# Kernel tuning notes

Measured on AMD Instinct MI355X. Metric: run time of the kernel, lower is better.

## Reference

```python
import jax, jax.numpy as jnp
import numpy as np

HEADS = 4
HID = 32
IN_CH = 3
N = 50000
E = 800000


def setup_inputs() -> dict:
    key = jax.random.key(0)
    ks = jax.random.split(key, 16)
    d1 = HEADS * HID  # 128
    s = 0.1
    inp = {
        'x': jax.random.normal(ks[0], (N, IN_CH), jnp.float32),
        'edge_index': jax.random.randint(ks[1], (2, E), 0, N, jnp.int64),
        # layer 1: in=3 -> heads*hid
        'W1': jax.random.normal(ks[2], (IN_CH, d1), jnp.float32) * s,
        'as1': jax.random.normal(ks[3], (HEADS, HID), jnp.float32) * s,
        'ad1': jax.random.normal(ks[4], (HEADS, HID), jnp.float32) * s,
        'b1': jnp.zeros((d1,), jnp.float32),
        # layer 2: 128 -> 128
        'W2': jax.random.normal(ks[5], (d1, d1), jnp.float32) * s,
        'as2': jax.random.normal(ks[6], (HEADS, HID), jnp.float32) * s,
        'ad2': jax.random.normal(ks[7], (HEADS, HID), jnp.float32) * s,
        'b2': jnp.zeros((d1,), jnp.float32),
        # layer 3: 128 -> 128
        'W3': jax.random.normal(ks[8], (d1, d1), jnp.float32) * s,
        'as3': jax.random.normal(ks[9], (HEADS, HID), jnp.float32) * s,
        'ad3': jax.random.normal(ks[10], (HEADS, HID), jnp.float32) * s,
        'b3': jnp.zeros((d1,), jnp.float32),
        # classifier: 128 -> 1
        'cW': jax.random.normal(ks[11], (d1, 1), jnp.float32) * s,
        'cb': jnp.zeros((1,), jnp.float32),
    }
    return inp


def _gat_layer(x, src, dst, n, W, a_s, a_d, b):
    """PyG GATConv (concat=True, negative_slope=0.2, self-loops already added)."""
    xp = (x @ W).reshape(n, HEADS, HID)              # [N,H,C]
    al_s = jnp.einsum('nhc,hc->nh', xp, a_s)          # [N,H]
    al_d = jnp.einsum('nhc,hc->nh', xp, a_d)          # [N,H]
    e = jax.nn.leaky_relu(al_s[src] + al_d[dst], 0.2)  # [E',H]
    emax = jax.ops.segment_max(e, dst, num_segments=n)  # segment softmax over dst
    ex = jnp.exp(e - emax[dst])
    den = jax.ops.segment_sum(ex, dst, num_segments=n)
    alpha = ex / (den[dst] + 1e-16)                   # [E',H]
    msg = xp[src] * alpha[:, :, None]                 # [E',H,C]
    out = jax.ops.segment_sum(msg, dst, num_segments=n)  # [N,H,C]
    return out.reshape(n, HEADS * HID) + b


def reference(x, edge_index, W1, as1, ad1, b1, W2, as2, ad2, b2, W3, as3, ad3, b3, cW, cb):
    n = x.shape[0]
    loops = jnp.arange(n, dtype=edge_index.dtype)
    src = jnp.concatenate([edge_index[0], loops])     # add self-loops (PyG default)
    dst = jnp.concatenate([edge_index[1], loops])
    h = jax.nn.elu(_gat_layer(x, src, dst, n, W1, as1, ad1, b1))
    h = jax.nn.elu(_gat_layer(h, src, dst, n, W2, as2, ad2, b2))
    h = jax.nn.elu(_gat_layer(h, src, dst, n, W3, as3, ad3, b3))
    logits = (h @ cW + cb)[:, 0]                      # [N]
    return jax.nn.sigmoid(logits)                     # eval mode output
```

## Files before the change

kernel.cpp:

```cpp
#include <hip/hip_runtime.h>
#include <math.h>

typedef unsigned int uint_t;
typedef __attribute__((ext_vector_type(8))) short bf16x8;
typedef __attribute__((ext_vector_type(4))) float f32x4;

#define BK_SHIFT 7
#define BK_NODES 128
#define MAXBK 512
#define PART_CHUNK 4096
#define SLAB 4096

__device__ __forceinline__ float lrelu(float x){ return x > 0.f ? x : 0.2f*x; }
__device__ __forceinline__ float sel4(float a, float b, float c, float d, int h){
    return h==0 ? a : (h==1 ? b : (h==2 ? c : d));
}
__device__ __forceinline__ float wsum(float v){
    #pragma unroll
    for (int m = 1; m < 64; m <<= 1) v += __shfl_xor(v, m);
    return v;
}
__device__ __forceinline__ uint_t pack_bf2(float a, float b){
    uint_t ua = __float_as_uint(a); uint_t ub = __float_as_uint(b);
    ua += 0x7FFFu + ((ua >> 16) & 1u);
    ub += 0x7FFFu + ((ub >> 16) & 1u);
    return (ua >> 16) | (ub & 0xFFFF0000u);
}
__device__ __forceinline__ float bflo(uint_t u){ return __uint_as_float(u << 16); }
__device__ __forceinline__ float bfhi(uint_t u){ return __uint_as_float(u & 0xFFFF0000u); }
__device__ __forceinline__ bf16x8 mk_bf8(uint4 u){
    bf16x8 r;
    r[0]=(short)(u.x & 0xFFFFu); r[1]=(short)(u.x >> 16);
    r[2]=(short)(u.y & 0xFFFFu); r[3]=(short)(u.y >> 16);
    r[4]=(short)(u.z & 0xFFFFu); r[5]=(short)(u.z >> 16);
    r[6]=(short)(u.w & 0xFFFFu); r[7]=(short)(u.w >> 16);
    return r;
}

__global__ __launch_bounds__(256) void wpack_zero(
        const float* __restrict__ W2, const float* __restrict__ W3,
        uint_t* __restrict__ B2, uint_t* __restrict__ B3,
        int* __restrict__ gcursor){
    int idx = blockIdx.x * 256 + threadIdx.x;
    if (idx < MAXBK) gcursor[idx] = 0;
    const float* W = (idx < 8192) ? W2 : W3;
    uint_t* Bp = (idx < 8192) ? B2 : B3;
    int i = idx & 8191;
    int u = i & 3, c = (i >> 2) & 15, kg = (i >> 6) & 3, kb = (i >> 8) & 3, cb = (i >> 10) & 7;
    int k = kb * 32 + kg * 8 + 2 * u;
    int col = cb * 16 + c;
    Bp[i] = pack_bf2(W[k * 128 + col], W[(k + 1) * 128 + col]);
}


__global__ __launch_bounds__(256) void partition_slab(
        const int* __restrict__ ei, int E, int N,
        int* __restrict__ gcursor, uint_t* __restrict__ pairbuf, int NBK){
    __shared__ int hist[MAXBK];
    __shared__ int sA[MAXBK];
    __shared__ int destadj[MAXBK];
    __shared__ int cnt2[MAXBK];
    __shared__ uint_t staged[PART_CHUNK];
    __shared__ unsigned short sbk[PART_CHUNK];
    int t = threadIdx.x;
    int base = blockIdx.x * PART_CHUNK;
    int total = E + N;
    int cnt = total - base; if (cnt > PART_CHUNK) cnt = PART_CHUNK; if (cnt < 0) cnt = 0;

    int sreg[16], dreg[16];
    #pragma unroll
    for (int q = 0; q < 16; ++q){
        int i = t + q * 256;
        int idx = base + i;
        int s = 0, d = -1;
        if (i < cnt){
            if (idx < E){ s = ei[idx]; d = ei[E + idx]; }
            else        { s = d = idx - E; }
        }
        sreg[q] = s; dreg[q] = d;
    }

    for (int i = t; i < MAXBK; i += 256){ hist[i] = 0; cnt2[i] = 0; }
    __syncthreads();
    #pragma unroll
    for (int q = 0; q < 16; ++q)
        if (dreg[q] >= 0) atomicAdd(&hist[dreg[q] >> BK_SHIFT], 1);
    __syncthreads();
    sA[t] = hist[t]; sA[t + 256] = hist[t + 256];
    __syncthreads();
    for (int off = 1; off < MAXBK; off <<= 1){
        int i0 = t, i1 = t + 256;
        int a0 = sA[i0] + ((i0 >= off) ? sA[i0 - off] : 0);
        int a1 = sA[i1] + ((i1 >= off) ? sA[i1 - off] : 0);
        __syncthreads();
        sA[i0] = a0; sA[i1] = a1;
        __syncthreads();
    }
    for (int b = t; b < NBK; b += 256){
        int c = hist[b];
        int gstart = (b == 0) ? 0 : sA[b - 1];
        int rbase = c > 0 ? atomicAdd(&gcursor[b], c) : 0;
        destadj[b] = b * SLAB + rbase - gstart;
        cnt2[b] = gstart;
    }
    __syncthreads();
    #pragma unroll
    for (int q = 0; q < 16; ++q){
        if (dreg[q] >= 0){
            int b = dreg[q] >> BK_SHIFT;
            int pos = atomicAdd(&cnt2[b], 1);
            staged[pos] = (uint_t)sreg[q] | ((uint_t)(dreg[q] & (BK_NODES - 1)) << 25);
            sbk[pos] = (unsigned short)b;
        }
    }
    __syncthreads();
    for (int p = t; p < cnt; p += 256){
        int b = (int)sbk[p];
        pairbuf[destadj[b] + p] = staged[p];
    }
}

__global__ __launch_bounds__(256) void sort2_slab(
        const uint_t* __restrict__ pairbuf, const int* __restrict__ gcursor,
        int* __restrict__ indptr, int* __restrict__ indend,
        int* __restrict__ srcs, int N, int NBK){
    int b = blockIdx.x;
    int cnt = gcursor[b];
    int base = b * SLAB;
    int nb = b << BK_SHIFT;
    __shared__ int nh[BK_NODES];
    __shared__ int noff[BK_NODES];
    __shared__ int outb[SLAB];
    int t = threadIdx.x;
    if (t < BK_NODES) nh[t] = 0;
    __syncthreads();
    for (int i = t; i < cnt; i += 256){
        uint_t pr = pairbuf[base + i];
        atomicAdd(&nh[(int)(pr >> 25)], 1);
    }
    __syncthreads();
    if (t < BK_NODES) noff[t] = nh[t];
    __syncthreads();
    for (int off = 1; off < BK_NODES; off <<= 1){
        int u = 0;
        if (t < BK_NODES && t >= off) u = noff[t - off];
        __syncthreads();
        if (t < BK_NODES) noff[t] += u;
        __syncthreads();
    }
    if (t < BK_NODES){
        int node = nb + t;
        if (node < N){
            int excl = noff[t] - nh[t];
            indptr[node] = base + excl;
            indend[node] = base + noff[t];
        }
        nh[t] = noff[t] - nh[t];
    }
    __syncthreads();
    for (int i = t; i < cnt; i += 256){
        uint_t pr = pairbuf[base + i];
        int pos = atomicAdd(&nh[(int)(pr >> 25)], 1);
        outb[pos] = (int)(pr & 0x1FFFFFFu);
    }
    __syncthreads();
    for (int i = t; i < cnt; i += 256) srcs[base + i] = outb[i];
}

__global__ __launch_bounds__(128) void linear_al(
        const float* __restrict__ in, const float* __restrict__ W,
        const float* __restrict__ as_, const float* __restrict__ ad_,
        uint_t* __restrict__ xp16, float* __restrict__ als, float* __restrict__ ald,
        int N, int K){
    __shared__ float hs[8 * 3];
    int t = threadIdx.x;
    int base = blockIdx.x * 8;
    int rows = N - base; if (rows > 8) rows = 8;
    for (int idx = t; idx < rows * K; idx += 128){
        int r = idx / K, k = idx - r * K;
        hs[r * K + k] = in[(size_t)(base + r) * K + k];
    }
    __syncthreads();
    float acc[8] = {0.f,0.f,0.f,0.f,0.f,0.f,0.f,0.f};
    for (int k = 0; k < K; ++k){
        float w = W[k * 128 + t];
        #pragma unroll
        for (int r = 0; r < 8; ++r) acc[r] += hs[r * K + k] * w;
    }
    float asv = as_[t], adv = ad_[t];
    for (int r = 0; r < rows; ++r){
        int row = base + r;
        float v = acc[r];
        float vo = __shfl_xor(v, 1);
        if (!(t & 1)) xp16[(size_t)row * 64 + (t >> 1)] = pack_bf2(v, vo);
        float vs = v * asv, vd = v * adv;
        #pragma unroll
        for (int m = 16; m >= 1; m >>= 1){
            vs += __shfl_xor(vs, m);
            vd += __shfl_xor(vd, m);
        }
        if ((t & 31) == 0){
            int h = t >> 5;
            als[row * 4 + h] = vs;
            ald[row * 4 + h] = vd;
        }
    }
}

__global__ __launch_bounds__(256) void gemm_mfma(
        const uint_t* __restrict__ h16, const uint_t* __restrict__ bpack,
        const float* __restrict__ as_, const float* __restrict__ ad_,
        uint_t* __restrict__ xp16, float* __restrict__ als, float* __restrict__ ald,
        int N){
    __shared__ uint4 Bs[2048];
    int t = threadIdx.x;
    const uint4* bp4 = (const uint4*)bpack;
    #pragma unroll
    for (int q = 0; q < 8; ++q) Bs[t + q * 256] = bp4[t + q * 256];
    __syncthreads();

    int w = threadIdx.x >> 6;
    int l = threadIdx.x & 63;
    int stripe = blockIdx.x * 4 + w;
    int base = stripe * 16;
    if (base >= N) return;
    int r16 = l & 15;
    int kg  = l >> 4;
    int row = base + r16;
    int rowc = row < N ? row : N - 1;

    bf16x8 afr[4];
    const uint4* hrow = (const uint4*)(h16 + (size_t)rowc * 64);
    #pragma unroll
    for (int kb = 0; kb < 4; ++kb) afr[kb] = mk_bf8(hrow[kb * 4 + kg]);

    f32x4 acc[8];
    #pragma unroll
    for (int cb = 0; cb < 8; ++cb) acc[cb] = (f32x4){0.f, 0.f, 0.f, 0.f};

    #pragma unroll
    for (int cb = 0; cb < 8; ++cb){
        #pragma unroll
        for (int kb = 0; kb < 4; ++kb){
            bf16x8 bfr = mk_bf8(Bs[((cb * 4 + kb) * 4 + kg) * 16 + r16]);
            acc[cb] = __builtin_amdgcn_mfma_f32_16x16x32_bf16(afr[kb], bfr, acc[cb], 0, 0, 0);
        }
    }

    #pragma unroll
    for (int reg = 0; reg < 4; ++reg){
        int ro = base + kg * 4 + reg;
        bool wr = (ro < N) && ((r16 & 1) == 0);
        #pragma unroll
        for (int cb = 0; cb < 8; ++cb){
            float v  = acc[cb][reg];
            float vo = __shfl_xor(v, 1);
            if (wr) xp16[(size_t)ro * 64 + cb * 8 + (r16 >> 1)] = pack_bf2(v, vo);
        }
        #pragma unroll
        for (int h = 0; h < 4; ++h){
            float a0 = as_[h * 32 + r16],      a1 = as_[h * 32 + 16 + r16];
            float g0 = ad_[h * 32 + r16],      g1 = ad_[h * 32 + 16 + r16];
            float ps = acc[2 * h][reg] * a0 + acc[2 * h + 1][reg] * a1;
            float pd = acc[2 * h][reg] * g0 + acc[2 * h + 1][reg] * g1;
            ps += __shfl_xor(ps, 1); ps += __shfl_xor(ps, 2);
            ps += __shfl_xor(ps, 4); ps += __shfl_xor(ps, 8);
            pd += __shfl_xor(pd, 1); pd += __shfl_xor(pd, 2);
            pd += __shfl_xor(pd, 4); pd += __shfl_xor(pd, 8);
            if (r16 == 0 && ro < N){
                als[(size_t)ro * 4 + h] = ps;
                ald[(size_t)ro * 4 + h] = pd;
            }
        }
    }
}

__global__ __launch_bounds__(256, 8) void gat_agg4(
        const uint_t* __restrict__ xp16, const float4* __restrict__ als,
        const float4* __restrict__ ald,
        const int* __restrict__ indptr, const int* __restrict__ indend,
        const int* __restrict__ srcs,
        const float* __restrict__ bias,
        uint_t* __restrict__ hout, int N, int mode,
        const float* __restrict__ cW, const float* __restrict__ cb,
        float* __restrict__ fout){
    int wid = threadIdx.x >> 6;
    int l   = threadIdx.x & 63;
    int n = blockIdx.x * 4 + wid;
    __shared__ int   ssh[4][64];
    __shared__ float esh[4][64][4];
    if (n >= N) return;

    int beg = indptr[n], end = indend[n];
    float4 ad4 = ald[n];
    int h = l >> 4;

    float d0 = 0.f, d1 = 0.f, d2 = 0.f, d3 = 0.f;
    float ax = 0.f, ay = 0.f;

    for (int cbeg = beg; cbeg < end; cbeg += 64){
        int cnt = end - cbeg; if (cnt > 64) cnt = 64;
        if (l < cnt){
            int s = srcs[cbeg + l];
            ssh[wid][l] = s;
            float4 a4 = als[s];
            float p0 = __expf(lrelu(a4.x + ad4.x));
            float p1 = __expf(lrelu(a4.y + ad4.y));
            float p2 = __expf(lrelu(a4.z + ad4.z));
            float p3 = __expf(lrelu(a4.w + ad4.w));
            *((float4*)&esh[wid][l][0]) = make_float4(p0, p1, p2, p3);
            d0 += p0; d1 += p1; d2 += p2; d3 += p3;
        }
        __builtin_amdgcn_wave_barrier();

        int j = 0;
        for (; j + 16 <= cnt; j += 16){
            int ss[16]; float ww[16]; uint_t uu[16];
            #pragma unroll
            for (int q = 0; q < 16; ++q){ ss[q] = ssh[wid][j+q]; ww[q] = esh[wid][j+q][h]; }
            #pragma unroll
            for (int q = 0; q < 16; ++q) uu[q] = xp16[(size_t)ss[q] * 64 + l];
            #pragma unroll
            for (int q = 0; q < 16; ++q){
                ax = fmaf(bflo(uu[q]), ww[q], ax);
                ay = fmaf(bfhi(uu[q]), ww[q], ay);
            }
        }
        for (; j + 8 <= cnt; j += 8){
            int ss[8]; float ww[8]; uint_t uu[8];
            #pragma unroll
            for (int q = 0; q < 8; ++q){ ss[q] = ssh[wid][j+q]; ww[q] = esh[wid][j+q][h]; }
            #pragma unroll
            for (int q = 0; q < 8; ++q) uu[q] = xp16[(size_t)ss[q] * 64 + l];
            #pragma unroll
            for (int q = 0; q < 8; ++q){
                ax = fmaf(bflo(uu[q]), ww[q], ax);
                ay = fmaf(bfhi(uu[q]), ww[q], ay);
            }
        }
        for (; j < cnt; ++j){
            int s = ssh[wid][j];
            float w = esh[wid][j][h];
            uint_t u = xp16[(size_t)s * 64 + l];
            ax = fmaf(bflo(u), w, ax);
            ay = fmaf(bfhi(u), w, ay);
        }
    }

    d0 = wsum(d0); d1 = wsum(d1); d2 = wsum(d2); d3 = wsum(d3);

    float dh = sel4(d0, d1, d2, d3, h);
    float inv = 1.f / (dh + 1e-16f);
    float2 b2 = ((const float2*)bias)[l];
    float vx = ax * inv + b2.x;
    float vy = ay * inv + b2.y;
    vx = vx > 0.f ? vx : (__expf(vx) - 1.f);
    vy = vy > 0.f ? vy : (__expf(vy) - 1.f);

    if (mode == 0){
        hout[(size_t)n * 64 + l] = pack_bf2(vx, vy);
    } else {
        float2 cw2 = ((const float2*)cW)[l];
        float p = vx * cw2.x + vy * cw2.y;
        p = wsum(p);
        if (l == 0){
            float logit = p + cb[0];
            fout[n] = 1.f / (1.f + __expf(-logit));
        }
    }
}

extern "C" void kernel_launch(void* const* d_in, const int* in_sizes, int n_in,
                              void* d_out, int out_size, void* d_ws, size_t ws_size,
                              hipStream_t stream){
    const float* x   = (const float*)d_in[0];
    const int*   ei  = (const int*)d_in[1];
    const float* W1  = (const float*)d_in[2];
    const float* as1 = (const float*)d_in[3];
    const float* ad1 = (const float*)d_in[4];
    const float* b1  = (const float*)d_in[5];
    const float* W2  = (const float*)d_in[6];
    const float* as2 = (const float*)d_in[7];
    const float* ad2 = (const float*)d_in[8];
    const float* b2  = (const float*)d_in[9];
    const float* W3  = (const float*)d_in[10];
    const float* as3 = (const float*)d_in[11];
    const float* ad3 = (const float*)d_in[12];
    const float* b3  = (const float*)d_in[13];
    const float* cW  = (const float*)d_in[14];
    const float* cb  = (const float*)d_in[15];
    float* out = (float*)d_out;

    int N = in_sizes[0] / 3;
    int E = in_sizes[1] / 2;
    int EN = E + N;
    int NBK = (N + BK_NODES - 1) / BK_NODES;

    char* ws = (char*)d_ws;
    size_t off = 0;
    auto alloc = [&](size_t bytes) -> void* {
        void* p = ws + off;
        off += (bytes + 255) & ~(size_t)255;
        return p;
    };
    int*    indptr  = (int*)alloc((size_t)N * 4);
    int*    indend  = (int*)alloc((size_t)N * 4);
    int*    srcs    = (int*)alloc((size_t)NBK * SLAB * 4);
    uint_t* pairbuf = (uint_t*)alloc((size_t)NBK * SLAB * 4);
    uint_t* XP      = (uint_t*)alloc((size_t)N * 64 * 4);
    uint_t* H16     = (uint_t*)alloc((size_t)N * 64 * 4);
    float*  ALS     = (float*)alloc((size_t)N * 4 * 4);
    float*  ALD     = (float*)alloc((size_t)N * 4 * 4);
    int*    gcursor = (int*)alloc((size_t)MAXBK * 4);
    uint_t* BP2     = (uint_t*)alloc((size_t)8192 * 4);
    uint_t* BP3     = (uint_t*)alloc((size_t)8192 * 4);
    (void)ws_size;

    int pb = (EN + PART_CHUNK - 1) / PART_CHUNK;

    wpack_zero<<<64, 256, 0, stream>>>(W2, W3, BP2, BP3, gcursor);
    partition_slab<<<pb, 256, 0, stream>>>(ei, E, N, gcursor, pairbuf, NBK);
    sort2_slab<<<NBK, 256, 0, stream>>>(pairbuf, gcursor, indptr, indend, srcs, N, NBK);

    int ab = (N + 3) / 4;
    int gb = ((N + 15) / 16 + 3) / 4;
    linear_al<<<(N + 7) / 8, 128, 0, stream>>>(x, W1, as1, ad1, XP, ALS, ALD, N, 3);
    gat_agg4<<<ab, 256, 0, stream>>>(XP, (const float4*)ALS, (const float4*)ALD,
                                     indptr, indend, srcs, b1, H16, N, 0, nullptr, nullptr, nullptr);
    gemm_mfma<<<gb, 256, 0, stream>>>(H16, BP2, as2, ad2, XP, ALS, ALD, N);
    gat_agg4<<<ab, 256, 0, stream>>>(XP, (const float4*)ALS, (const float4*)ALD,
                                     indptr, indend, srcs, b2, H16, N, 0, nullptr, nullptr, nullptr);
    gemm_mfma<<<gb, 256, 0, stream>>>(H16, BP3, as3, ad3, XP, ALS, ALD, N);
    gat_agg4<<<ab, 256, 0, stream>>>(XP, (const float4*)ALS, (const float4*)ALD,
                                     indptr, indend, srcs, b3, nullptr, N, 1, cW, cb, out);
}
```

Measured before the change: 206.5 us.

## Split GAT aggregation per head with 16-lane node groups and separate classifier

```diff
diff --git a/kernel.cpp b/kernel.cpp
--- a/kernel.cpp
+++ b/kernel.cpp
@@ -12,9 +12,6 @@
 #define SLAB 4096
 
 __device__ __forceinline__ float lrelu(float x){ return x > 0.f ? x : 0.2f*x; }
-__device__ __forceinline__ float sel4(float a, float b, float c, float d, int h){
-    return h==0 ? a : (h==1 ? b : (h==2 ? c : d));
-}
 __device__ __forceinline__ float wsum(float v){
     #pragma unroll
     for (int m = 1; m < 64; m <<= 1) v += __shfl_xor(v, m);
@@ -275,99 +272,68 @@
     }
 }
 
-__global__ __launch_bounds__(256, 8) void gat_agg4(
-        const uint_t* __restrict__ xp16, const float4* __restrict__ als,
-        const float4* __restrict__ ald,
+__global__ __launch_bounds__(256, 8) void gat_agg5(
+        const uint_t* __restrict__ xp16, const float* __restrict__ als,
+        const float* __restrict__ ald,
         const int* __restrict__ indptr, const int* __restrict__ indend,
-        const int* __restrict__ srcs,
-        const float* __restrict__ bias,
-        uint_t* __restrict__ hout, int N, int mode,
-        const float* __restrict__ cW, const float* __restrict__ cb,
-        float* __restrict__ fout){
-    int wid = threadIdx.x >> 6;
-    int l   = threadIdx.x & 63;
-    int n = blockIdx.x * 4 + wid;
-    __shared__ int   ssh[4][64];
-    __shared__ float esh[4][64][4];
+        const int* __restrict__ srcs, const float* __restrict__ bias,
+        uint_t* __restrict__ hout, int N){
+    int bid = blockIdx.x;
+    int h     = (bid & 7) >> 1;
+    int chunk = (bid >> 3) * 2 + (bid & 1);
+    int wid  = threadIdx.x >> 6;
+    int lane = threadIdx.x & 63;
+    int g = lane >> 4, l16 = lane & 15;
+    int n = chunk * 16 + wid * 4 + g;
     if (n >= N) return;
 
     int beg = indptr[n], end = indend[n];
-    float4 ad4 = ald[n];
-    int h = l >> 4;
-
-    float d0 = 0.f, d1 = 0.f, d2 = 0.f, d3 = 0.f;
-    float ax = 0.f, ay = 0.f;
-
-    for (int cbeg = beg; cbeg < end; cbeg += 64){
-        int cnt = end - cbeg; if (cnt > 64) cnt = 64;
-        if (l < cnt){
-            int s = srcs[cbeg + l];
-            ssh[wid][l] = s;
-            float4 a4 = als[s];
-            float p0 = __expf(lrelu(a4.x + ad4.x));
-            float p1 = __expf(lrelu(a4.y + ad4.y));
-            float p2 = __expf(lrelu(a4.z + ad4.z));
-            float p3 = __expf(lrelu(a4.w + ad4.w));
-            *((float4*)&esh[wid][l][0]) = make_float4(p0, p1, p2, p3);
-            d0 += p0; d1 += p1; d2 += p2; d3 += p3;
-        }
-        __builtin_amdgcn_wave_barrier();
-
-        int j = 0;
-        for (; j + 16 <= cnt; j += 16){
-            int ss[16]; float ww[16]; uint_t uu[16];
-            #pragma unroll
-            for (int q = 0; q < 16; ++q){ ss[q] = ssh[wid][j+q]; ww[q] = esh[wid][j+q][h]; }
-            #pragma unroll
-            for (int q = 0; q < 16; ++q) uu[q] = xp16[(size_t)ss[q] * 64 + l];
-            #pragma unroll
-            for (int q = 0; q < 16; ++q){
-                ax = fmaf(bflo(uu[q]), ww[q], ax);
-                ay = fmaf(bfhi(uu[q]), ww[q], ay);
+    float adh = ald[n * 4 + h];
+    float d = 0.f, ax = 0.f, ay = 0.f;
+    int gbase = g * 16;
+
+    for (int cbeg = beg; cbeg < end; cbeg += 16){
+        int cnt = end - cbeg; if (cnt > 16) cnt = 16;
+        int s = 0; float w = 0.f;
+        if (l16 < cnt){
+            s = __builtin_nontemporal_load(&srcs[cbeg + l16]);
+            w = __expf(lrelu(als[s * 4 + h] + adh));
+            d += w;
+        }
+        #pragma unroll
+        for (int e = 0; e < 16; ++e){
+            int   se = __shfl(s, gbase + e);
+            float we = __shfl(w, gbase + e);
+            if (e < cnt){
+                uint_t u = xp16[(size_t)se * 64 + h * 16 + l16];
+                ax = fmaf(bflo(u), we, ax);
+                ay = fmaf(bfhi(u), we, ay);
             }
         }
-        for (; j + 8 <= cnt; j += 8){
-            int ss[8]; float ww[8]; uint_t uu[8];
-            #pragma unroll
-            for (int q = 0; q < 8; ++q){ ss[q] = ssh[wid][j+q]; ww[q] = esh[wid][j+q][h]; }
-            #pragma unroll
-            for (int q = 0; q < 8; ++q) uu[q] = xp16[(size_t)ss[q] * 64 + l];
-            #pragma unroll
-            for (int q = 0; q < 8; ++q){
-                ax = fmaf(bflo(uu[q]), ww[q], ax);
-                ay = fmaf(bfhi(uu[q]), ww[q], ay);
-            }
-        }
-        for (; j < cnt; ++j){
-            int s = ssh[wid][j];
-            float w = esh[wid][j][h];
-            uint_t u = xp16[(size_t)s * 64 + l];
-            ax = fmaf(bflo(u), w, ax);
-            ay = fmaf(bfhi(u), w, ay);
-        }
-    }
-
-    d0 = wsum(d0); d1 = wsum(d1); d2 = wsum(d2); d3 = wsum(d3);
-
-    float dh = sel4(d0, d1, d2, d3, h);
-    float inv = 1.f / (dh + 1e-16f);
-    float2 b2 = ((const float2*)bias)[l];
+    }
+
+    d += __shfl_xor(d, 1); d += __shfl_xor(d, 2);
+    d += __shfl_xor(d, 4); d += __shfl_xor(d, 8);
+    float inv = 1.f / (d + 1e-16f);
+    float2 b2 = ((const float2*)bias)[h * 16 + l16];
     float vx = ax * inv + b2.x;
     float vy = ay * inv + b2.y;
     vx = vx > 0.f ? vx : (__expf(vx) - 1.f);
     vy = vy > 0.f ? vy : (__expf(vy) - 1.f);
-
-    if (mode == 0){
-        hout[(size_t)n * 64 + l] = pack_bf2(vx, vy);
-    } else {
-        float2 cw2 = ((const float2*)cW)[l];
-        float p = vx * cw2.x + vy * cw2.y;
-        p = wsum(p);
-        if (l == 0){
-            float logit = p + cb[0];
-            fout[n] = 1.f / (1.f + __expf(-logit));
-        }
-    }
+    hout[(size_t)n * 64 + h * 16 + l16] = pack_bf2(vx, vy);
+}
+
+__global__ __launch_bounds__(256, 8) void classifier_kernel(
+        const uint_t* __restrict__ h16, const float* __restrict__ cW,
+        const float* __restrict__ cb, float* __restrict__ fout, int N){
+    int n = blockIdx.x * 4 + (threadIdx.x >> 6);
+    int l = threadIdx.x & 63;
+    if (n >= N) return;
+    uint_t u = h16[(size_t)n * 64 + l];
+    float2 cw2 = ((const float2*)cW)[l];
+    float p = bflo(u) * cw2.x + bfhi(u) * cw2.y;
+    p = wsum(p);
+    if (l == 0) fout[n] = 1.f / (1.f + __expf(-(p + cb[0])));
 }
 
 extern "C" void kernel_launch(void* const* d_in, const int* in_sizes, int n_in,
@@ -422,15 +388,14 @@
     partition_slab<<<pb, 256, 0, stream>>>(ei, E, N, gcursor, pairbuf, NBK);
     sort2_slab<<<NBK, 256, 0, stream>>>(pairbuf, gcursor, indptr, indend, srcs, N, NBK);
 
-    int ab = (N + 3) / 4;
+    int chunks = (N + 15) / 16;
+    int a5 = ((chunks + 1) / 2) * 8;
     int gb = ((N + 15) / 16 + 3) / 4;
     linear_al<<<(N + 7) / 8, 128, 0, stream>>>(x, W1, as1, ad1, XP, ALS, ALD, N, 3);
-    gat_agg4<<<ab, 256, 0, stream>>>(XP, (const float4*)ALS, (const float4*)ALD,
-                                     indptr, indend, srcs, b1, H16, N, 0, nullptr, nullptr, nullptr);
+    gat_agg5<<<a5, 256, 0, stream>>>(XP, ALS, ALD, indptr, indend, srcs, b1, H16, N);
     gemm_mfma<<<gb, 256, 0, stream>>>(H16, BP2, as2, ad2, XP, ALS, ALD, N);
-    gat_agg4<<<ab, 256, 0, stream>>>(XP, (const float4*)ALS, (const float4*)ALD,
-                                     indptr, indend, srcs, b2, H16, N, 0, nullptr, nullptr, nullptr);
+    gat_agg5<<<a5, 256, 0, stream>>>(XP, ALS, ALD, indptr, indend, srcs, b2, H16, N);
     gemm_mfma<<<gb, 256, 0, stream>>>(H16, BP3, as3, ad3, XP, ALS, ALD, N);
-    gat_agg4<<<ab, 256, 0, stream>>>(XP, (const float4*)ALS, (const float4*)ALD,
-                                     indptr, indend, srcs, b3, nullptr, N, 1, cW, cb, out);
-}
+    gat_agg5<<<a5, 256, 0, stream>>>(XP, ALS, ALD, indptr, indend, srcs, b3, H16, N);
+    classifier_kernel<<<(N + 3) / 4, 256, 0, stream>>>(H16, cW, cb, out, N);
+}
```

Result: slower. 355.0 us (+71.9%).
